# Performance work log

Measured on AMD Instinct MI355X. Metric: run time of the kernel, lower is better.

## Reference

```python
import jax, jax.numpy as jnp
import numpy as np

D_MODEL = 1024
N_HEADS = 16
N_KV = 8
GROUP = N_HEADS // N_KV  # 2
D_HEAD = D_MODEL // N_HEADS  # 64
SCALE = D_HEAD ** -0.5


def setup_inputs() -> dict:
    key = jax.random.key(0)
    ks = jax.random.split(key, 5)
    s = 0.02
    return {
        "x": jax.random.normal(ks[0], (2, 2048, D_MODEL), dtype=jnp.float32),
        "Wq": jax.random.normal(ks[1], (D_MODEL, D_MODEL), dtype=jnp.float32) * s,
        "Wk": jax.random.normal(ks[2], (N_KV * D_HEAD, D_MODEL), dtype=jnp.float32) * s,
        "Wv": jax.random.normal(ks[3], (N_KV * D_HEAD, D_MODEL), dtype=jnp.float32) * s,
        "Wproj": jax.random.normal(ks[4], (D_MODEL, D_MODEL), dtype=jnp.float32) * s,
    }


def reference(x, Wq, Wk, Wv, Wproj):
    b, t, c = x.shape
    # projections (torch Linear: x @ W.T)
    q = (x @ Wq.T).reshape(b, t, N_KV, GROUP, D_HEAD)  # heads ordered (kv, group)
    k = (x @ Wk.T).reshape(b, t, N_KV, D_HEAD)
    v = (x @ Wv.T).reshape(b, t, N_KV, D_HEAD)
    # repeat_interleave(K/V, group, dim=heads) == broadcast over the group axis,
    # since q head index h maps to kv head h // GROUP.
    scores = jnp.einsum('btkgd,bskd->bkgts', q, k) * SCALE  # (b, kv, g, t, s)
    attn = jax.nn.softmax(scores, axis=-1)
    y = jnp.einsum('bkgts,bskd->btkgd', attn, v)  # (b, t, kv, g, d)
    y = y.reshape(b, t, c)
    return y @ Wproj.T
```

## Files before the change

### kernel.cpp

```cpp
#include <hip/hip_runtime.h>


#define SEQ    2048
#define CDIM   1024
#define KVDIM  512
#define SCL2E  0.18033688011112042f

typedef __attribute__((ext_vector_type(8))) short   bf16x8;
typedef __attribute__((ext_vector_type(4))) float   f32x4;
typedef unsigned short ushort_t;

__device__ __forceinline__ ushort_t f2bf(float f) {
    unsigned u = __float_as_uint(f);
    u += 0x7FFFu + ((u >> 16) & 1u);
    return (ushort_t)(u >> 16);
}
__device__ __forceinline__ float bf2f(ushort_t h) {
    return __uint_as_float(((unsigned)h) << 16);
}
__device__ __forceinline__ void load_lds16(const void* g, void* l) {
    __builtin_amdgcn_global_load_lds(
        (const __attribute__((address_space(1))) void*)g,
        (__attribute__((address_space(3))) void*)l, 16, 0, 0);
}

__global__ __launch_bounds__(256) void cvt_bf16(
    const float* __restrict__ x,  const float* __restrict__ wq,
    const float* __restrict__ wk, const float* __restrict__ wv,
    const float* __restrict__ wp,
    ushort_t* __restrict__ xh,  ushort_t* __restrict__ wqh,
    ushort_t* __restrict__ wkh, ushort_t* __restrict__ wvh,
    ushort_t* __restrict__ wph)
{
    const int i = blockIdx.x * 256 + threadIdx.x;
    const float* src; ushort_t* dst; int off;
    if (i < 1048576)      { src = x;  dst = xh;  off = i; }
    else if (i < 1310720) { src = wq; dst = wqh; off = i - 1048576; }
    else if (i < 1441792) { src = wk; dst = wkh; off = i - 1310720; }
    else if (i < 1572864) { src = wv; dst = wvh; off = i - 1441792; }
    else                  { src = wp; dst = wph; off = i - 1572864; }
    const float4 v = ((const float4*)src)[off];
    ushort4 h;
    h.x = f2bf(v.x); h.y = f2bf(v.y); h.z = f2bf(v.z); h.w = f2bf(v.w);
    ((ushort4*)dst)[off] = h;
}

__global__ __launch_bounds__(256, 4) void gemm64(
    const ushort_t* __restrict__ A, int K,
    const ushort_t* __restrict__ B1, void* __restrict__ C1, int N1, int epi1, float sc1,
    const ushort_t* __restrict__ B2, void* __restrict__ C2, int N2, int epi2, float sc2,
    const ushort_t* __restrict__ B3, void* __restrict__ C3, int N3, int epi3, float sc3)
{
    __shared__ ushort_t sA[128 * 64];
    __shared__ ushort_t sB[64 * 64];

    const int tid = threadIdx.x, wv = tid >> 6, lane = tid & 63;
    const int lm = lane & 15, quad = lane >> 4;
    const int m0 = blockIdx.y * 128;

    const int t1 = N1 >> 6, t2 = N2 >> 6;
    const int bx = blockIdx.x;
    const ushort_t* B; void* Cv; int n0, Nout, epi; float sc;
    if (bx < t1)           { B = B1; Cv = C1; Nout = N1; epi = epi1; sc = sc1; n0 = bx * 64; }
    else if (bx < t1 + t2) { B = B2; Cv = C2; Nout = N2; epi = epi2; sc = sc2; n0 = (bx - t1) * 64; }
    else                   { B = B3; Cv = C3; Nout = N3; epi = epi3; sc = sc3; n0 = (bx - t1 - t2) * 64; }

    const int mh = wv >> 1, nh = wv & 1;
    const int srow = lane >> 3;
    const int scol = ((lane & 7) ^ ((lane >> 3) & 7)) * 8;

    f32x4 acc[4][2] = {};

    for (int k0 = 0; k0 < K; k0 += 64) {
        __syncthreads();
        #pragma unroll
        for (int i = 0; i < 6; ++i) {
            const int g = wv * 6 + i;
            if (g < 16)
                load_lds16(A + (size_t)(m0 + g * 8 + srow) * K + k0 + scol, sA + g * 512);
            else
                load_lds16(B + (size_t)(n0 + (g - 16) * 8 + srow) * K + k0 + scol, sB + (g - 16) * 512);
        }
        __syncthreads();

        #pragma unroll
        for (int ks = 0; ks < 2; ++ks) {
            const int co = ((ks * 4 + quad) ^ (lm & 7)) * 8;
            bf16x8 a[4], b[2];
            #pragma unroll
            for (int mt = 0; mt < 4; ++mt)
                a[mt] = *(const bf16x8*)&sA[(mh * 64 + mt * 16 + lm) * 64 + co];
            #pragma unroll
            for (int nt = 0; nt < 2; ++nt)
                b[nt] = *(const bf16x8*)&sB[(nh * 32 + nt * 16 + lm) * 64 + co];
            #pragma unroll
            for (int mt = 0; mt < 4; ++mt)
                #pragma unroll
                for (int nt = 0; nt < 2; ++nt)
                    acc[mt][nt] = __builtin_amdgcn_mfma_f32_16x16x32_bf16(a[mt], b[nt], acc[mt][nt], 0, 0, 0);
        }
    }

    if (epi == 0) {
        float* C = (float*)Cv;
        #pragma unroll
        for (int mt = 0; mt < 4; ++mt)
            #pragma unroll
            for (int nt = 0; nt < 2; ++nt)
                #pragma unroll
                for (int r = 0; r < 4; ++r)
                    C[(size_t)(m0 + mh * 64 + mt * 16 + quad * 4 + r) * Nout + n0 + nh * 32 + nt * 16 + lm]
                        = acc[mt][nt][r];
    } else {
        ushort_t* C = (ushort_t*)Cv;
        #pragma unroll
        for (int mt = 0; mt < 4; ++mt)
            #pragma unroll
            for (int nt = 0; nt < 2; ++nt)
                #pragma unroll
                for (int r = 0; r < 4; ++r)
                    C[(size_t)(m0 + mh * 64 + mt * 16 + quad * 4 + r) * Nout + n0 + nh * 32 + nt * 16 + lm]
                        = f2bf(acc[mt][nt][r] * sc);
    }
}

__global__ __launch_bounds__(256) void vtrans_kernel(
    const float* __restrict__ v, ushort_t* __restrict__ vt)
{
    __shared__ float tile[64][65];
    const int t0  = blockIdx.x * 64;
    const int bkv = blockIdx.y;
    const int r   = threadIdx.x >> 2;
    const int c0  = (threadIdx.x & 3) * 16;

    const float* src = v + (size_t)((bkv >> 3) * SEQ + t0 + r) * KVDIM + (bkv & 7) * 64 + c0;
    #pragma unroll
    for (int i = 0; i < 4; ++i) {
        const float4 f = *(const float4*)(src + i * 4);
        tile[r][c0 + i*4 + 0] = f.x;
        tile[r][c0 + i*4 + 1] = f.y;
        tile[r][c0 + i*4 + 2] = f.z;
        tile[r][c0 + i*4 + 3] = f.w;
    }
    __syncthreads();
    ushort_t* dst = vt + (size_t)(bkv * 64 + r) * SEQ + t0 + c0;
    #pragma unroll
    for (int i = 0; i < 4; ++i) {
        ushort4 u;
        u.x = f2bf(tile[c0 + i*4 + 0][r]);
        u.y = f2bf(tile[c0 + i*4 + 1][r]);
        u.z = f2bf(tile[c0 + i*4 + 2][r]);
        u.w = f2bf(tile[c0 + i*4 + 3][r]);
        *(ushort4*)(dst + i * 4) = u;
    }
}

__global__ __launch_bounds__(256, 2) void attn4(
    const ushort_t* __restrict__ Qh, const ushort_t* __restrict__ Kh,
    const ushort_t* __restrict__ Vth, ushort_t* __restrict__ Yh)
{
    __shared__ ushort_t sK[2][64 * 64];
    __shared__ ushort_t sV[2][64 * 64];
    __shared__ ushort_t sP[4 * 2048];

    const int tid = threadIdx.x, wv = tid >> 6, lane = tid & 63;
    const int lm = lane & 15, quad = lane >> 4;
    const int b = blockIdx.y >> 4, h = blockIdx.y & 15, kvh = h >> 1;
    const int t0 = blockIdx.x * 128, tq0 = t0 + wv * 32;

    bf16x8 qh[2][2];
    #pragma unroll
    for (int qg = 0; qg < 2; ++qg) {
        const size_t rb = (size_t)(b * SEQ + tq0 + qg * 16 + lm) * CDIM + h * 64;
        #pragma unroll
        for (int ks = 0; ks < 2; ++ks)
            qh[qg][ks] = *(const bf16x8*)(Qh + rb + ks * 32 + quad * 8);
    }

    const ushort_t* gK = Kh  + (size_t)b * SEQ * KVDIM + kvh * 64;
    const ushort_t* gV = Vth + (size_t)(b * 8 + kvh) * 64 * SEQ;
    ushort_t* pw = sP + wv * 2048;

    const int sit  = (wv & 1) * 4;
    const int srow = lane >> 3;
    const int scol = ((lane & 7) ^ ((lane >> 3) & 7)) * 8;

    float l_r[2] = {0.0f, 0.0f};
    f32x4 O[2][4] = {};

    if (wv < 2) {
        #pragma unroll
        for (int it = 0; it < 4; ++it)
            load_lds16(gK + (size_t)((sit + it) * 8 + srow) * KVDIM + scol,
                       &sK[0][(sit + it) * 512]);
    } else {
        #pragma unroll
        for (int it = 0; it < 4; ++it)
            load_lds16(gV + (size_t)((sit + it) * 8 + srow) * SEQ + scol,
                       &sV[0][(sit + it) * 512]);
    }

    for (int kt = 0; kt < SEQ / 64; ++kt) {
        const int cur = kt & 1;
        __syncthreads();

        if (kt + 1 < SEQ / 64) {
            const int s1 = (kt + 1) * 64;
            if (wv < 2) {
                #pragma unroll
                for (int it = 0; it < 4; ++it)
                    load_lds16(gK + (size_t)(s1 + (sit + it) * 8 + srow) * KVDIM + scol,
                               &sK[cur ^ 1][(sit + it) * 512]);
            } else {
                #pragma unroll
                for (int it = 0; it < 4; ++it)
                    load_lds16(gV + (size_t)((sit + it) * 8 + srow) * SEQ + s1 + scol,
                               &sV[cur ^ 1][(sit + it) * 512]);
            }
        }

        f32x4 st[2][4] = {};
        #pragma unroll
        for (int sti = 0; sti < 4; ++sti)
            #pragma unroll
            for (int ks = 0; ks < 2; ++ks) {
                const int off = (sti * 16 + lm) * 64 + (((ks * 4 + quad) ^ (lm & 7)) * 8);
                const bf16x8 kf = *(const bf16x8*)&sK[cur][off];
                #pragma unroll
                for (int qg = 0; qg < 2; ++qg)
                    st[qg][sti] = __builtin_amdgcn_mfma_f32_16x16x32_bf16(kf, qh[qg][ks], st[qg][sti], 0, 0, 0);
            }

        #pragma unroll
        for (int qg = 0; qg < 2; ++qg)
            #pragma unroll
            for (int sti = 0; sti < 4; ++sti) {
                const float p0 = __builtin_amdgcn_exp2f(st[qg][sti][0]);
                const float p1 = __builtin_amdgcn_exp2f(st[qg][sti][1]);
                const float p2 = __builtin_amdgcn_exp2f(st[qg][sti][2]);
                const float p3 = __builtin_amdgcn_exp2f(st[qg][sti][3]);
                l_r[qg] += (p0 + p1) + (p2 + p3);
                uint2 u;
                u.x = __builtin_amdgcn_perm(__float_as_uint(p1), __float_as_uint(p0), 0x07060302u);
                u.y = __builtin_amdgcn_perm(__float_as_uint(p3), __float_as_uint(p2), 0x07060302u);
                const int off = (qg * 16 + lm) * 64
                              + (((sti * 2 + (quad >> 1)) ^ (lm & 7)) * 8) + (quad & 1) * 4;
                *(uint2*)&pw[off] = u;
            }
        __asm__ volatile("s_waitcnt lgkmcnt(0)" ::: "memory");

        #pragma unroll
        for (int ks = 0; ks < 2; ++ks) {
            const int co = ((ks * 4 + quad) ^ (lm & 7)) * 8;
            bf16x8 pa[2];
            #pragma unroll
            for (int qg = 0; qg < 2; ++qg)
                pa[qg] = *(const bf16x8*)&pw[(qg * 16 + lm) * 64 + co];
            #pragma unroll
            for (int dt = 0; dt < 4; ++dt) {
                const bf16x8 vt = *(const bf16x8*)&sV[cur][(dt * 16 + lm) * 64 + co];
                #pragma unroll
                for (int qg = 0; qg < 2; ++qg)
                    O[qg][dt] = __builtin_amdgcn_mfma_f32_16x16x32_bf16(pa[qg], vt, O[qg][dt], 0, 0, 0);
            }
        }
    }

    #pragma unroll
    for (int qg = 0; qg < 2; ++qg) {
        l_r[qg] += __shfl_xor(l_r[qg], 16);
        l_r[qg] += __shfl_xor(l_r[qg], 32);
    }
    #pragma unroll
    for (int qg = 0; qg < 2; ++qg)
        #pragma unroll
        for (int r = 0; r < 4; ++r) {
            const float lq = __shfl(l_r[qg], (lane & 48) | (quad * 4 + r));
            const float inv = 1.0f / lq;
            const int t = tq0 + qg * 16 + quad * 4 + r;
            const size_t rowb = (size_t)(b * SEQ + t) * CDIM + h * 64;
            #pragma unroll
            for (int dt = 0; dt < 4; ++dt)
                Yh[rowb + dt * 16 + lm] = f2bf(O[qg][dt][r] * inv);
        }
}

extern "C" void kernel_launch(void* const* d_in, const int* in_sizes, int n_in,
                              void* d_out, int out_size, void* d_ws, size_t ws_size,
                              hipStream_t stream)
{
    const float* x     = (const float*)d_in[0];
    const float* Wq    = (const float*)d_in[1];
    const float* Wk    = (const float*)d_in[2];
    const float* Wv    = (const float*)d_in[3];
    const float* Wproj = (const float*)d_in[4];
    float* out = (float*)d_out;

    const int M = 2 * SEQ;

    char* p = (char*)d_ws;
    ushort_t* xh   = (ushort_t*)p; p += (size_t)M * CDIM * 2;
    ushort_t* wqh  = (ushort_t*)p; p += (size_t)CDIM * CDIM * 2;
    ushort_t* wkh  = (ushort_t*)p; p += (size_t)KVDIM * CDIM * 2;
    ushort_t* wvh  = (ushort_t*)p; p += (size_t)KVDIM * CDIM * 2;
    ushort_t* wph  = (ushort_t*)p; p += (size_t)CDIM * CDIM * 2;
    ushort_t* qh   = (ushort_t*)p; p += (size_t)M * CDIM * 2;
    ushort_t* kh   = (ushort_t*)p; p += (size_t)M * KVDIM * 2;
    float*    vbuf = (float*)p;    p += (size_t)M * KVDIM * 4;
    ushort_t* vth  = (ushort_t*)p; p += (size_t)M * KVDIM * 2;
    ushort_t* yh = xh;

    dim3 blk(256);

    cvt_bf16<<<dim3(7168), blk, 0, stream>>>(
        x, Wq, Wk, Wv, Wproj, xh, wqh, wkh, wvh, wph);

    gemm64<<<dim3(32, 32), blk, 0, stream>>>(
        xh, CDIM,
        wqh, qh,   CDIM,  3, SCL2E,
        wkh, kh,   KVDIM, 3, 1.0f,
        wvh, vbuf, KVDIM, 0, 1.0f);

    vtrans_kernel<<<dim3(SEQ / 64, 16), blk, 0, stream>>>(vbuf, vth);

    attn4<<<dim3(SEQ / 128, 32), blk, 0, stream>>>(qh, kh, vth, yh);

    gemm64<<<dim3(16, 32), blk, 0, stream>>>(
        yh, CDIM,
        wph, out, CDIM, 0, 1.0f,
        nullptr, nullptr, 0, 0, 1.0f,
        nullptr, nullptr, 0, 0, 1.0f);
}
```

Measured before the change: 167.9 us.

## Double-buffer GEMM tiles and widen attention waves to 64 query rows

Result: slower. 201.8 us (+20.2%).

```diff
diff --git a/kernel.cpp b/kernel.cpp
--- a/kernel.cpp
+++ b/kernel.cpp
@@ -45,14 +45,14 @@
     ((ushort4*)dst)[off] = h;
 }
 
-__global__ __launch_bounds__(256, 4) void gemm64(
+__global__ __launch_bounds__(256, 3) void gemm64(
     const ushort_t* __restrict__ A, int K,
     const ushort_t* __restrict__ B1, void* __restrict__ C1, int N1, int epi1, float sc1,
     const ushort_t* __restrict__ B2, void* __restrict__ C2, int N2, int epi2, float sc2,
     const ushort_t* __restrict__ B3, void* __restrict__ C3, int N3, int epi3, float sc3)
 {
-    __shared__ ushort_t sA[128 * 64];
-    __shared__ ushort_t sB[64 * 64];
+    __shared__ ushort_t sA[2][128 * 64];
+    __shared__ ushort_t sB[2][64 * 64];
 
     const int tid = threadIdx.x, wv = tid >> 6, lane = tid & 63;
     const int lm = lane & 15, quad = lane >> 4;
@@ -71,17 +71,31 @@
 
     f32x4 acc[4][2] = {};
 
-    for (int k0 = 0; k0 < K; k0 += 64) {
+    #pragma unroll
+    for (int i = 0; i < 6; ++i) {
+        const int g = wv * 6 + i;
+        if (g < 16)
+            load_lds16(A + (size_t)(m0 + g * 8 + srow) * K + scol, &sA[0][g * 512]);
+        else
+            load_lds16(B + (size_t)(n0 + (g - 16) * 8 + srow) * K + scol, &sB[0][(g - 16) * 512]);
+    }
+
+    const int iters = K >> 6;
+    for (int it = 0; it < iters; ++it) {
+        const int cur = it & 1;
         __syncthreads();
-        #pragma unroll
-        for (int i = 0; i < 6; ++i) {
-            const int g = wv * 6 + i;
-            if (g < 16)
-                load_lds16(A + (size_t)(m0 + g * 8 + srow) * K + k0 + scol, sA + g * 512);
-            else
-                load_lds16(B + (size_t)(n0 + (g - 16) * 8 + srow) * K + k0 + scol, sB + (g - 16) * 512);
-        }
-        __syncthreads();
+
+        if (it + 1 < iters) {
+            const int k1 = (it + 1) * 64;
+            #pragma unroll
+            for (int i = 0; i < 6; ++i) {
+                const int g = wv * 6 + i;
+                if (g < 16)
+                    load_lds16(A + (size_t)(m0 + g * 8 + srow) * K + k1 + scol, &sA[cur ^ 1][g * 512]);
+                else
+                    load_lds16(B + (size_t)(n0 + (g - 16) * 8 + srow) * K + k1 + scol, &sB[cur ^ 1][(g - 16) * 512]);
+            }
+        }
 
         #pragma unroll
         for (int ks = 0; ks < 2; ++ks) {
@@ -89,10 +103,10 @@
             bf16x8 a[4], b[2];
             #pragma unroll
             for (int mt = 0; mt < 4; ++mt)
-                a[mt] = *(const bf16x8*)&sA[(mh * 64 + mt * 16 + lm) * 64 + co];
+                a[mt] = *(const bf16x8*)&sA[cur][(mh * 64 + mt * 16 + lm) * 64 + co];
             #pragma unroll
             for (int nt = 0; nt < 2; ++nt)
-                b[nt] = *(const bf16x8*)&sB[(nh * 32 + nt * 16 + lm) * 64 + co];
+                b[nt] = *(const bf16x8*)&sB[cur][(nh * 32 + nt * 16 + lm) * 64 + co];
             #pragma unroll
             for (int mt = 0; mt < 4; ++mt)
                 #pragma unroll
@@ -155,49 +169,46 @@
     }
 }
 
-__global__ __launch_bounds__(256, 2) void attn4(
+__global__ __launch_bounds__(128, 2) void attn5(
     const ushort_t* __restrict__ Qh, const ushort_t* __restrict__ Kh,
     const ushort_t* __restrict__ Vth, ushort_t* __restrict__ Yh)
 {
     __shared__ ushort_t sK[2][64 * 64];
     __shared__ ushort_t sV[2][64 * 64];
-    __shared__ ushort_t sP[4 * 2048];
+    __shared__ ushort_t sP[2][64 * 64];
 
     const int tid = threadIdx.x, wv = tid >> 6, lane = tid & 63;
     const int lm = lane & 15, quad = lane >> 4;
     const int b = blockIdx.y >> 4, h = blockIdx.y & 15, kvh = h >> 1;
-    const int t0 = blockIdx.x * 128, tq0 = t0 + wv * 32;
-
-    bf16x8 qh[2][2];
-    #pragma unroll
-    for (int qg = 0; qg < 2; ++qg) {
+    const int t0 = blockIdx.x * 128, tq0 = t0 + wv * 64;
+
+    bf16x8 qf[4][2];
+    #pragma unroll
+    for (int qg = 0; qg < 4; ++qg) {
         const size_t rb = (size_t)(b * SEQ + tq0 + qg * 16 + lm) * CDIM + h * 64;
         #pragma unroll
         for (int ks = 0; ks < 2; ++ks)
-            qh[qg][ks] = *(const bf16x8*)(Qh + rb + ks * 32 + quad * 8);
+            qf[qg][ks] = *(const bf16x8*)(Qh + rb + ks * 32 + quad * 8);
     }
 
     const ushort_t* gK = Kh  + (size_t)b * SEQ * KVDIM + kvh * 64;
     const ushort_t* gV = Vth + (size_t)(b * 8 + kvh) * 64 * SEQ;
-    ushort_t* pw = sP + wv * 2048;
-
-    const int sit  = (wv & 1) * 4;
+    ushort_t* pw = sP[wv];
+
     const int srow = lane >> 3;
     const int scol = ((lane & 7) ^ ((lane >> 3) & 7)) * 8;
 
-    float l_r[2] = {0.0f, 0.0f};
-    f32x4 O[2][4] = {};
-
-    if (wv < 2) {
-        #pragma unroll
-        for (int it = 0; it < 4; ++it)
-            load_lds16(gK + (size_t)((sit + it) * 8 + srow) * KVDIM + scol,
-                       &sK[0][(sit + it) * 512]);
+    float l_r[4] = {};
+    f32x4 O[4][4] = {};
+
+    if (wv == 0) {
+        #pragma unroll
+        for (int it = 0; it < 8; ++it)
+            load_lds16(gK + (size_t)(it * 8 + srow) * KVDIM + scol, &sK[0][it * 512]);
     } else {
         #pragma unroll
-        for (int it = 0; it < 4; ++it)
-            load_lds16(gV + (size_t)((sit + it) * 8 + srow) * SEQ + scol,
-                       &sV[0][(sit + it) * 512]);
+        for (int it = 0; it < 8; ++it)
+            load_lds16(gV + (size_t)(it * 8 + srow) * SEQ + scol, &sV[0][it * 512]);
     }
 
     for (int kt = 0; kt < SEQ / 64; ++kt) {
@@ -206,20 +217,20 @@
 
         if (kt + 1 < SEQ / 64) {
             const int s1 = (kt + 1) * 64;
-            if (wv < 2) {
-                #pragma unroll
-                for (int it = 0; it < 4; ++it)
-                    load_lds16(gK + (size_t)(s1 + (sit + it) * 8 + srow) * KVDIM + scol,
-                               &sK[cur ^ 1][(sit + it) * 512]);
+            if (wv == 0) {
+                #pragma unroll
+                for (int it = 0; it < 8; ++it)
+                    load_lds16(gK + (size_t)(s1 + it * 8 + srow) * KVDIM + scol,
+                               &sK[cur ^ 1][it * 512]);
             } else {
                 #pragma unroll
-                for (int it = 0; it < 4; ++it)
-                    load_lds16(gV + (size_t)((sit + it) * 8 + srow) * SEQ + s1 + scol,
-                               &sV[cur ^ 1][(sit + it) * 512]);
-            }
-        }
-
-        f32x4 st[2][4] = {};
+                for (int it = 0; it < 8; ++it)
+                    load_lds16(gV + (size_t)(it * 8 + srow) * SEQ + s1 + scol,
+                               &sV[cur ^ 1][it * 512]);
+            }
+        }
+
+        f32x4 st[4][4] = {};
         #pragma unroll
         for (int sti = 0; sti < 4; ++sti)
             #pragma unroll
@@ -227,12 +238,12 @@
                 const int off = (sti * 16 + lm) * 64 + (((ks * 4 + quad) ^ (lm & 7)) * 8);
                 const bf16x8 kf = *(const bf16x8*)&sK[cur][off];
                 #pragma unroll
-                for (int qg = 0; qg < 2; ++qg)
-                    st[qg][sti] = __builtin_amdgcn_mfma_f32_16x16x32_bf16(kf, qh[qg][ks], st[qg][sti], 0, 0, 0);
-            }
-
-        #pragma unroll
-        for (int qg = 0; qg < 2; ++qg)
+                for (int qg = 0; qg < 4; ++qg)
+                    st[qg][sti] = __builtin_amdgcn_mfma_f32_16x16x32_bf16(kf, qf[qg][ks], st[qg][sti], 0, 0, 0);
+            }
+
+        #pragma unroll
+        for (int qg = 0; qg < 4; ++qg)
             #pragma unroll
             for (int sti = 0; sti < 4; ++sti) {
                 const float p0 = __builtin_amdgcn_exp2f(st[qg][sti][0]);
@@ -252,27 +263,27 @@
         #pragma unroll
         for (int ks = 0; ks < 2; ++ks) {
             const int co = ((ks * 4 + quad) ^ (lm & 7)) * 8;
-            bf16x8 pa[2];
-            #pragma unroll
-            for (int qg = 0; qg < 2; ++qg)
+            bf16x8 pa[4];
+            #pragma unroll
+            for (int qg = 0; qg < 4; ++qg)
                 pa[qg] = *(const bf16x8*)&pw[(qg * 16 + lm) * 64 + co];
             #pragma unroll
             for (int dt = 0; dt < 4; ++dt) {
                 const bf16x8 vt = *(const bf16x8*)&sV[cur][(dt * 16 + lm) * 64 + co];
                 #pragma unroll
-                for (int qg = 0; qg < 2; ++qg)
+                for (int qg = 0; qg < 4; ++qg)
                     O[qg][dt] = __builtin_amdgcn_mfma_f32_16x16x32_bf16(pa[qg], vt, O[qg][dt], 0, 0, 0);
             }
         }
     }
 
     #pragma unroll
-    for (int qg = 0; qg < 2; ++qg) {
+    for (int qg = 0; qg < 4; ++qg) {
         l_r[qg] += __shfl_xor(l_r[qg], 16);
         l_r[qg] += __shfl_xor(l_r[qg], 32);
     }
     #pragma unroll
-    for (int qg = 0; qg < 2; ++qg)
+    for (int qg = 0; qg < 4; ++qg)
         #pragma unroll
         for (int r = 0; r < 4; ++r) {
             const float lq = __shfl(l_r[qg], (lane & 48) | (quad * 4 + r));
@@ -323,7 +334,7 @@
 
     vtrans_kernel<<<dim3(SEQ / 64, 16), blk, 0, stream>>>(vbuf, vth);
 
-    attn4<<<dim3(SEQ / 128, 32), blk, 0, stream>>>(qh, kh, vth, yh);
+    attn5<<<dim3(SEQ / 128, 32), dim3(128), 0, stream>>>(qh, kh, vth, yh);
 
     gemm64<<<dim3(16, 32), blk, 0, stream>>>(
         yh, CDIM,
```

## Widen GEMM tiles to 128x128 and double-buffer LDS loads

Applied to the files above, without the earlier changes.

New measurement: 174.2 us. 3.7% more time.

```diff
diff --git a/kernel.cpp b/kernel.cpp
--- a/kernel.cpp
+++ b/kernel.cpp
@@ -45,58 +45,72 @@
     ((ushort4*)dst)[off] = h;
 }
 
-__global__ __launch_bounds__(256, 4) void gemm64(
+__global__ __launch_bounds__(256, 2) void gemm128db(
     const ushort_t* __restrict__ A, int K,
     const ushort_t* __restrict__ B1, void* __restrict__ C1, int N1, int epi1, float sc1,
     const ushort_t* __restrict__ B2, void* __restrict__ C2, int N2, int epi2, float sc2,
     const ushort_t* __restrict__ B3, void* __restrict__ C3, int N3, int epi3, float sc3)
 {
-    __shared__ ushort_t sA[128 * 64];
-    __shared__ ushort_t sB[64 * 64];
+    __shared__ ushort_t sA[2][128 * 64];
+    __shared__ ushort_t sB[2][128 * 64];
 
     const int tid = threadIdx.x, wv = tid >> 6, lane = tid & 63;
     const int lm = lane & 15, quad = lane >> 4;
     const int m0 = blockIdx.y * 128;
 
-    const int t1 = N1 >> 6, t2 = N2 >> 6;
+    const int t1 = N1 >> 7, t2 = N2 >> 7;
     const int bx = blockIdx.x;
     const ushort_t* B; void* Cv; int n0, Nout, epi; float sc;
-    if (bx < t1)           { B = B1; Cv = C1; Nout = N1; epi = epi1; sc = sc1; n0 = bx * 64; }
-    else if (bx < t1 + t2) { B = B2; Cv = C2; Nout = N2; epi = epi2; sc = sc2; n0 = (bx - t1) * 64; }
-    else                   { B = B3; Cv = C3; Nout = N3; epi = epi3; sc = sc3; n0 = (bx - t1 - t2) * 64; }
+    if (bx < t1)           { B = B1; Cv = C1; Nout = N1; epi = epi1; sc = sc1; n0 = bx * 128; }
+    else if (bx < t1 + t2) { B = B2; Cv = C2; Nout = N2; epi = epi2; sc = sc2; n0 = (bx - t1) * 128; }
+    else                   { B = B3; Cv = C3; Nout = N3; epi = epi3; sc = sc3; n0 = (bx - t1 - t2) * 128; }
 
     const int mh = wv >> 1, nh = wv & 1;
     const int srow = lane >> 3;
     const int scol = ((lane & 7) ^ ((lane >> 3) & 7)) * 8;
 
-    f32x4 acc[4][2] = {};
-
-    for (int k0 = 0; k0 < K; k0 += 64) {
+    f32x4 acc[4][4] = {};
+
+    #pragma unroll
+    for (int i = 0; i < 8; ++i) {
+        const int g = wv * 8 + i;
+        if (g < 16)
+            load_lds16(A + (size_t)(m0 + g * 8 + srow) * K + scol, &sA[0][g * 512]);
+        else
+            load_lds16(B + (size_t)(n0 + (g - 16) * 8 + srow) * K + scol, &sB[0][(g - 16) * 512]);
+    }
+
+    const int iters = K >> 6;
+    for (int it = 0; it < iters; ++it) {
+        const int cur = it & 1;
         __syncthreads();
-        #pragma unroll
-        for (int i = 0; i < 6; ++i) {
-            const int g = wv * 6 + i;
-            if (g < 16)
-                load_lds16(A + (size_t)(m0 + g * 8 + srow) * K + k0 + scol, sA + g * 512);
-            else
-                load_lds16(B + (size_t)(n0 + (g - 16) * 8 + srow) * K + k0 + scol, sB + (g - 16) * 512);
-        }
-        __syncthreads();
+
+        if (it + 1 < iters) {
+            const int k1 = (it + 1) * 64;
+            #pragma unroll
+            for (int i = 0; i < 8; ++i) {
+                const int g = wv * 8 + i;
+                if (g < 16)
+                    load_lds16(A + (size_t)(m0 + g * 8 + srow) * K + k1 + scol, &sA[cur ^ 1][g * 512]);
+                else
+                    load_lds16(B + (size_t)(n0 + (g - 16) * 8 + srow) * K + k1 + scol, &sB[cur ^ 1][(g - 16) * 512]);
+            }
+        }
 
         #pragma unroll
         for (int ks = 0; ks < 2; ++ks) {
             const int co = ((ks * 4 + quad) ^ (lm & 7)) * 8;
-            bf16x8 a[4], b[2];
+            bf16x8 a[4], b[4];
             #pragma unroll
             for (int mt = 0; mt < 4; ++mt)
-                a[mt] = *(const bf16x8*)&sA[(mh * 64 + mt * 16 + lm) * 64 + co];
-            #pragma unroll
-            for (int nt = 0; nt < 2; ++nt)
-                b[nt] = *(const bf16x8*)&sB[(nh * 32 + nt * 16 + lm) * 64 + co];
+                a[mt] = *(const bf16x8*)&sA[cur][(mh * 64 + mt * 16 + lm) * 64 + co];
+            #pragma unroll
+            for (int nt = 0; nt < 4; ++nt)
+                b[nt] = *(const bf16x8*)&sB[cur][(nh * 64 + nt * 16 + lm) * 64 + co];
             #pragma unroll
             for (int mt = 0; mt < 4; ++mt)
                 #pragma unroll
-                for (int nt = 0; nt < 2; ++nt)
+                for (int nt = 0; nt < 4; ++nt)
                     acc[mt][nt] = __builtin_amdgcn_mfma_f32_16x16x32_bf16(a[mt], b[nt], acc[mt][nt], 0, 0, 0);
         }
     }
@@ -106,20 +120,20 @@
         #pragma unroll
         for (int mt = 0; mt < 4; ++mt)
             #pragma unroll
-            for (int nt = 0; nt < 2; ++nt)
+            for (int nt = 0; nt < 4; ++nt)
                 #pragma unroll
                 for (int r = 0; r < 4; ++r)
-                    C[(size_t)(m0 + mh * 64 + mt * 16 + quad * 4 + r) * Nout + n0 + nh * 32 + nt * 16 + lm]
+                    C[(size_t)(m0 + mh * 64 + mt * 16 + quad * 4 + r) * Nout + n0 + nh * 64 + nt * 16 + lm]
                         = acc[mt][nt][r];
     } else {
         ushort_t* C = (ushort_t*)Cv;
         #pragma unroll
         for (int mt = 0; mt < 4; ++mt)
             #pragma unroll
-            for (int nt = 0; nt < 2; ++nt)
+            for (int nt = 0; nt < 4; ++nt)
                 #pragma unroll
                 for (int r = 0; r < 4; ++r)
-                    C[(size_t)(m0 + mh * 64 + mt * 16 + quad * 4 + r) * Nout + n0 + nh * 32 + nt * 16 + lm]
+                    C[(size_t)(m0 + mh * 64 + mt * 16 + quad * 4 + r) * Nout + n0 + nh * 64 + nt * 16 + lm]
                         = f2bf(acc[mt][nt][r] * sc);
     }
 }
@@ -315,7 +329,7 @@
     cvt_bf16<<<dim3(7168), blk, 0, stream>>>(
         x, Wq, Wk, Wv, Wproj, xh, wqh, wkh, wvh, wph);
 
-    gemm64<<<dim3(32, 32), blk, 0, stream>>>(
+    gemm128db<<<dim3(16, 32), blk, 0, stream>>>(
         xh, CDIM,
         wqh, qh,   CDIM,  3, SCL2E,
         wkh, kh,   KVDIM, 3, 1.0f,
@@ -325,7 +339,7 @@
 
     attn4<<<dim3(SEQ / 128, 32), blk, 0, stream>>>(qh, kh, vth, yh);
 
-    gemm64<<<dim3(16, 32), blk, 0, stream>>>(
+    gemm128db<<<dim3(8, 32), blk, 0, stream>>>(
         yh, CDIM,
         wph, out, CDIM, 0, 1.0f,
         nullptr, nullptr, 0, 0, 1.0f,
```
